# Kernel tuning notes

Measured on AMD Instinct MI355X. Metric: run time of the kernel, lower is better.

Reference implementation:

```python
import jax, jax.numpy as jnp
import numpy as np
import math

B, LL, LP, H, C, S, T = 16, 512, 2048, 1024, 8192, 10, 4
PAD_TOKEN_ID = 2000
VAR_TOKEN_BASE = 2001


def _attend(q, k, v):
    # q: [b,q,h], k/v: [b,k,h]
    scores = jnp.einsum('bqh,bkh->bqk', q, k) / math.sqrt(float(q.shape[-1]))
    w = jax.nn.softmax(scores, axis=-1)
    return jnp.einsum('bqk,bkh->bqh', w, v)


def _gru_cell(x, h, Wih, Whh, bih, bhh):
    gi = x @ Wih + bih   # [B,3H], gate order r,z,n (torch GRUCell)
    gh = h @ Whh + bhh
    i_r, i_z, i_n = jnp.split(gi, 3, axis=-1)
    h_r, h_z, h_n = jnp.split(gh, 3, axis=-1)
    r = jax.nn.sigmoid(i_r + h_r)
    z = jax.nn.sigmoid(i_z + h_z)
    n = jnp.tanh(i_n + r * h_n)
    return (1.0 - z) * n + z * h


def setup_inputs() -> dict:
    key = jax.random.key(0)
    ks = jax.random.split(key, 18)
    def lin(k, i, o):
        return jax.random.normal(k, (i, o), jnp.float32) * 0.02
    return {
        'logic_hidden': jax.random.normal(ks[0], (B, LL, H), jnp.float32),
        'prompt_hidden': jax.random.normal(ks[1], (B, LP, H), jnp.float32),
        'codebook_emb': jax.random.normal(ks[2], (C, H), jnp.float32) * 0.02,
        'W_init': lin(ks[3], 2 * H, H),
        'W_pq': lin(ks[4], H, H),
        'W_pk': lin(ks[5], H, H),
        'W_pv': lin(ks[6], H, H),
        'slot_queries': jax.random.normal(ks[7], (S - 1, H), jnp.float32) * 0.02,
        'W_sq': lin(ks[8], H, H),
        'W_op': lin(ks[9], H, H),
        'W_gate': lin(ks[10], H, 1),
        'b_gate': jnp.zeros((1,), jnp.float32),
        'W_stop': lin(ks[11], 2 * H, 1),
        'b_stop': jnp.zeros((1,), jnp.float32),
        'gru_Wih': lin(ks[12], H, 3 * H),
        'gru_Whh': lin(ks[13], H, 3 * H),
        'gru_bih': jnp.zeros((3 * H,), jnp.float32),
        'gru_bhh': jnp.zeros((3 * H,), jnp.float32),
    }


def reference(logic_hidden, prompt_hidden, codebook_emb, W_init, W_pq, W_pk, W_pv,
              slot_queries, W_sq, W_op, W_gate, b_gate, W_stop, b_stop,
              gru_Wih, gru_Whh, gru_bih, gru_bhh):
    batch = logic_hidden.shape[0]
    prompt_summary = prompt_hidden.mean(axis=1)
    logic_summary = logic_hidden.mean(axis=1)
    state = jnp.tanh(jnp.concatenate([prompt_summary, logic_summary], axis=-1) @ W_init)
    pk = prompt_hidden @ W_pk   # [B,LP,H]
    pv = prompt_hidden @ W_pv
    cb_sq = jnp.sum(codebook_emb * codebook_emb, axis=-1)   # [C]
    slot_idx = jnp.arange(S - 1, dtype=jnp.int64)[None, :].repeat(batch, axis=0)

    summaries, stop_logits, stop_probs = [], [], []
    for _ in range(T):
        state_q = (state @ W_pq)[:, None, :]
        state_ctx = _attend(state_q, pk, pv)[:, 0, :]         # [B,H]
        op_pre = state_ctx @ W_op
        # squared euclidean distance to codebook without [B,C,H] diff tensor
        dist = (jnp.sum(op_pre * op_pre, axis=-1, keepdims=True)
                - 2.0 * (op_pre @ codebook_emb.T) + cb_sq[None, :])  # [B,C]
        op_logits = -dist
        op_idx = jnp.argmax(op_logits, axis=-1)               # [B]
        op_embedding = codebook_emb[op_idx]                   # [B,H]
        slot_seed = state_ctx[:, None, :] + slot_queries[None, :, :]   # [B,S-1,H]
        slot_q = slot_seed @ W_sq
        slot_tensors = _attend(slot_q, pk, pv)                # [B,S-1,H]
        slot_use_probs = jax.nn.sigmoid((slot_seed @ W_gate)[..., 0] + b_gate[0])  # [B,S-1]
        slot_mask = slot_use_probs >= 0.5
        # fallback if no slot selected anywhere in the batch (global check, as in torch)
        fb_mask = jax.nn.one_hot(jnp.argmax(slot_use_probs, axis=-1), S - 1, dtype=jnp.bool_)
        slot_mask = jnp.where(jnp.any(slot_mask), slot_mask, fb_mask)
        mf = slot_mask.astype(slot_tensors.dtype)
        slot_summary = jnp.sum(slot_tensors * mf[..., None], axis=1) / \
            jnp.clip(jnp.sum(mf, axis=-1, keepdims=True), 1.0)
        matrix_summary = jnp.tanh(op_embedding + slot_summary)
        stop_logit = (jnp.concatenate([state_ctx, matrix_summary], axis=-1) @ W_stop)[:, 0] + b_stop[0]
        summaries.append(matrix_summary)
        stop_logits.append(stop_logit)
        stop_probs.append(jax.nn.sigmoid(stop_logit))
        state = _gru_cell(matrix_summary, state, gru_Wih, gru_Whh, gru_bih, gru_bhh)

    stop_logits_t = jnp.stack(stop_logits, axis=1)   # [B,T]
    stop_probs_t = jnp.stack(stop_probs, axis=1)
    summary_stack = jnp.stack(summaries, axis=1)     # [B,T,H]
    stop_hits = stop_probs_t >= 0.5
    chain_lengths = jnp.argmax(stop_hits.astype(jnp.int64), axis=1) + 1
    chain_lengths = jnp.where(jnp.sum(stop_hits, axis=1) == 0,
                              jnp.full_like(chain_lengths, T), chain_lengths)
    return summary_stack, stop_logits_t, stop_probs_t, chain_lengths
```

## Files before the change

kernel.cpp:

```cpp
#include <hip/hip_runtime.h>


#define DINL __device__ __forceinline__

DINL float dot4(float4 a, float4 b) {
  return fmaf(a.x, b.x, fmaf(a.y, b.y, fmaf(a.z, b.z, a.w * b.w)));
}
DINL unsigned sortable(float f) {
  unsigned u = __float_as_uint(f);
  return (u & 0x80000000u) ? ~u : (u | 0x80000000u);
}
#define AXPY4(A, W, P) \
  { A.x = fmaf(W, P.x, A.x); A.y = fmaf(W, P.y, A.y); A.z = fmaf(W, P.z, A.z); A.w = fmaf(W, P.w, A.w); }
#define ADD4(A, V) { A.x += V.x; A.y += V.y; A.z += V.z; A.w += V.w; }

static constexpr int F_CBSQ  = 0;
static constexpr int F_STATE = 8192;
static constexpr int F_WQK   = 24576;
static constexpr int F_T1    = F_WQK + 1048576;
static constexpr int F_WFUSE = F_T1 + 1048576;
static constexpr int F_SQKCP = F_WFUSE + 2105344;
static constexpr int F_E     = F_SQKCP + 36928;
static constexpr int F_UN    = F_E + 294912;
static constexpr int F_PMP   = F_UN;
static constexpr int F_LMP   = F_PMP + 1048576;
static constexpr int F_MEAN  = F_LMP + 262144;
static constexpr int F_S2P   = F_MEAN + 32768;
static constexpr int F_WQKP  = F_UN;
static constexpr int F_T1P   = F_UN + 4194304;
static constexpr int F_WFP   = F_UN;
static constexpr int F_QS1   = F_UN;
static constexpr int F_LST   = F_QS1 + 131072;
static constexpr int F_CTX   = F_LST + 4096;
static constexpr int F_FWP   = F_CTX + 16384;
static constexpr int F_OPV   = F_FWP + 1052672;
static constexpr int F_OPMAX = F_OPV + 16384;
static constexpr int F_OPIDX = F_OPMAX + 16384;
static constexpr int F_GPRE  = F_OPIDX + 64;
static constexpr int F_GC    = F_GPRE + 64;
static constexpr int F_STOPA = F_GC + 64;
static constexpr int F_QSLB  = F_STOPA + 64;
static constexpr int F_LPS   = F_QSLB + 16384;
static constexpr int F_SSUM  = F_LPS + 4672;
static constexpr int F_MS    = F_SSUM + 16384;
static constexpr int F_GP    = F_MS + 16384;
static constexpr int F_K8P   = F_GP + 786432;
static constexpr int F_BIG   = F_K8P + 262144;

struct SG {
  const float* Bm;
  const float* Bg;
  const float* a0;
  float* out;
  int M, N, Ncore, NB, kslice, ksh, lda, ldb, ldo, mr;
  float scale;
};

template <int MR>
DINL void sgemm_body(const SG p, int bx, float* As) {
  const int t = threadIdx.x;
  const int ks = bx / p.NB, nb = bx % p.NB;
  const int kslice = p.kslice;
  const int kb = ks * kslice;
  const int tot = p.M * kslice;
  for (int idx = t; idx < tot; idx += 256) {
    const int m = idx >> p.ksh;
    const int kl = idx & (kslice - 1);
    As[(m << p.ksh) + kl] = p.a0[m * p.lda + kb + kl];
  }
  __syncthreads();
  const int nl = t & 63, mg = t >> 6;
  const int n = nb * 64 + nl;
  const bool nok = (n < p.N);
  float acc[MR];
#pragma unroll
  for (int i = 0; i < MR; i++) acc[i] = 0.f;
  const bool useg = nok && (n >= p.Ncore);
  const float* Bc = p.Bm + n;
  for (int k4 = 0; k4 < kslice; k4 += 4) {
    float bv[4];
#pragma unroll
    for (int u = 0; u < 4; u++) {
      bv[u] = 0.f;
      if (nok) bv[u] = useg ? p.Bg[kb + k4 + u] : Bc[(kb + k4 + u) * p.ldb];
    }
#pragma unroll
    for (int i = 0; i < MR; i++) {
      const int m = mg + 4 * i;
      if (MR == 4 || m < p.M) {
        const float4 av = *(const float4*)&As[(m << p.ksh) + k4];
        acc[i] = fmaf(av.x, bv[0], acc[i]);
        acc[i] = fmaf(av.y, bv[1], acc[i]);
        acc[i] = fmaf(av.z, bv[2], acc[i]);
        acc[i] = fmaf(av.w, bv[3], acc[i]);
      }
    }
  }
  if (nok) {
#pragma unroll
    for (int i = 0; i < MR; i++) {
      const int m = mg + 4 * i;
      if (MR == 4 || m < p.M) p.out[(ks * p.M + m) * p.ldo + n] = acc[i] * p.scale;
    }
  }
}

__global__ __launch_bounds__(256) void k_sgemm(SG p) {
  __shared__ __align__(16) float As[4352];
  if (p.mr == 4) sgemm_body<4>(p, blockIdx.x, As);
  else sgemm_body<7>(p, blockIdx.x, As);
}

DINL int sw4(int c) { return c ^ (((c >> 5) & 3) << 2); }

__global__ __launch_bounds__(256) void k_wgT(const float* __restrict__ A1,
                                             const float* __restrict__ B,
                                             float* __restrict__ C1P,
                                             const float* __restrict__ A2,
                                             float* __restrict__ C2P) {
  __shared__ __align__(16) float As[16 * 132], Bs[16 * 132];
  const int bx = blockIdx.x;
  const int which = bx >> 8;
  const int rem = bx & 255;
  const int ks = rem >> 6;
  const int tile = rem & 63;
  const int bi = tile >> 3, bj = tile & 7;
  const float* A = which ? A2 : A1;
  float* CP = (which ? C2P : C1P) + ks * 1048576;
  const int t = threadIdx.x;
  const int sr = t >> 2, q4 = t & 3;
  const int tr = (t >> 4) << 3, tc = (t & 15) << 3;
  const int stc0 = sw4(tc), stc1 = sw4(tc + 4);
  float acc[8][8];
#pragma unroll
  for (int i = 0; i < 8; i++)
#pragma unroll
    for (int j = 0; j < 8; j++) acc[i][j] = 0.f;

  const int k00 = ks * 256;
  for (int k0 = k00; k0 < k00 + 256; k0 += 16) {
    __syncthreads();
#pragma unroll
    for (int h = 0; h < 2; h++) {
      const int r = sr + h * 64;
      const float4 av = *(const float4*)&A[(bi * 128 + r) * 1024 + k0 + q4 * 4];
      const float4 bv = *(const float4*)&B[(bj * 128 + r) * 1024 + k0 + q4 * 4];
      As[(q4 * 4 + 0) * 132 + r] = av.x; As[(q4 * 4 + 1) * 132 + r] = av.y;
      As[(q4 * 4 + 2) * 132 + r] = av.z; As[(q4 * 4 + 3) * 132 + r] = av.w;
      const int swr = sw4(r);
      Bs[(q4 * 4 + 0) * 132 + swr] = bv.x; Bs[(q4 * 4 + 1) * 132 + swr] = bv.y;
      Bs[(q4 * 4 + 2) * 132 + swr] = bv.z; Bs[(q4 * 4 + 3) * 132 + swr] = bv.w;
    }
    __syncthreads();
#pragma unroll
    for (int kk = 0; kk < 16; kk++) {
      const float* ar = &As[kk * 132];
      const float* br = &Bs[kk * 132];
      const float4 a0 = *(const float4*)&ar[tr];
      const float4 a1 = *(const float4*)&ar[tr + 4];
      const float4 b0 = *(const float4*)&br[stc0];
      const float4 b1 = *(const float4*)&br[stc1];
      const float a[8] = {a0.x, a0.y, a0.z, a0.w, a1.x, a1.y, a1.z, a1.w};
      const float b[8] = {b0.x, b0.y, b0.z, b0.w, b1.x, b1.y, b1.z, b1.w};
#pragma unroll
      for (int i = 0; i < 8; i++)
#pragma unroll
        for (int j = 0; j < 8; j++) acc[i][j] = fmaf(a[i], b[j], acc[i][j]);
    }
  }
#pragma unroll
  for (int i = 0; i < 8; i++) {
    const int row = bi * 128 + tr + i;
    *(float4*)&CP[row * 1024 + bj * 128 + tc] =
        make_float4(acc[i][0], acc[i][1], acc[i][2], acc[i][3]);
    *(float4*)&CP[row * 1024 + bj * 128 + tc + 4] =
        make_float4(acc[i][4], acc[i][5], acc[i][6], acc[i][7]);
  }
}

__global__ __launch_bounds__(256) void k_combT(const float* __restrict__ C1P,
                                               const float* __restrict__ C2P,
                                               float* __restrict__ C1,
                                               float* __restrict__ C2, float scale) {
  const int bx = blockIdx.x;
  const int half = bx >> 12;
  const int i = ((bx & 4095) << 8) + threadIdx.x;
  const float* src = half ? C2P : C1P;
  float s = 0.f;
#pragma unroll
  for (int ks = 0; ks < 4; ks++) s += src[ks * 1048576 + i];
  (half ? C2 : C1)[i] = s * scale;
}

__global__ __launch_bounds__(256) void k_wgF(const float* __restrict__ Wpv,
                                             const float* __restrict__ Wop,
                                             const float* __restrict__ T1,
                                             float* __restrict__ CfP) {
  __shared__ __align__(16) float As[16 * 132], Bs[16 * 132];
  const int bx = blockIdx.x;
  const int ks = bx >> 7;
  const int rem = bx & 127;
  const int bi = rem >> 4, bj = rem & 15;
  const float* Bsrc = (bj < 8) ? (Wop + bj * 128) : (T1 + (bj - 8) * 128);
  float* CP = CfP + ks * 2105344;
  const int t = threadIdx.x;
  const int sr = t >> 2, q4 = t & 3;
  const int kkq = t >> 4, c8 = (t & 15) << 3;
  const int tr = (t >> 4) << 3, tc = (t & 15) << 3;
  const int stc0 = sw4(tc), stc1 = sw4(tc + 4);
  float acc[8][8];
#pragma unroll
  for (int i = 0; i < 8; i++)
#pragma unroll
    for (int j = 0; j < 8; j++) acc[i][j] = 0.f;

  const int k00 = ks * 256;
  for (int k0 = k00; k0 < k00 + 256; k0 += 16) {
    __syncthreads();
#pragma unroll
    for (int h = 0; h < 2; h++) {
      const int r = sr + h * 64;
      const float4 av = *(const float4*)&Wpv[(bi * 128 + r) * 1024 + k0 + q4 * 4];
      As[(q4 * 4 + 0) * 132 + r] = av.x; As[(q4 * 4 + 1) * 132 + r] = av.y;
      As[(q4 * 4 + 2) * 132 + r] = av.z; As[(q4 * 4 + 3) * 132 + r] = av.w;
    }
    {
      const float4 v0 = *(const float4*)&Bsrc[(k0 + kkq) * 1024 + c8];
      const float4 v1 = *(const float4*)&Bsrc[(k0 + kkq) * 1024 + c8 + 4];
      *(float4*)&Bs[kkq * 132 + sw4(c8)] = v0;
      *(float4*)&Bs[kkq * 132 + sw4(c8 + 4)] = v1;
    }
    __syncthreads();
#pragma unroll
    for (int kk = 0; kk < 16; kk++) {
      const float* ar = &As[kk * 132];
      const float* br = &Bs[kk * 132];
      const float4 a0 = *(const float4*)&ar[tr];
      const float4 a1 = *(const float4*)&ar[tr + 4];
      const float4 b0 = *(const float4*)&br[stc0];
      const float4 b1 = *(const float4*)&br[stc1];
      const float a[8] = {a0.x, a0.y, a0.z, a0.w, a1.x, a1.y, a1.z, a1.w};
      const float b[8] = {b0.x, b0.y, b0.z, b0.w, b1.x, b1.y, b1.z, b1.w};
#pragma unroll
      for (int i = 0; i < 8; i++)
#pragma unroll
        for (int j = 0; j < 8; j++) acc[i][j] = fmaf(a[i], b[j], acc[i][j]);
    }
  }
#pragma unroll
  for (int i = 0; i < 8; i++) {
    const int row = bi * 128 + tr + i;
    *(float4*)&CP[row * 2056 + bj * 128 + tc] =
        make_float4(acc[i][0], acc[i][1], acc[i][2], acc[i][3]);
    *(float4*)&CP[row * 2056 + bj * 128 + tc + 4] =
        make_float4(acc[i][4], acc[i][5], acc[i][6], acc[i][7]);
  }
}

__global__ __launch_bounds__(256) void k_combF(const float* __restrict__ CfP,
                                               float* __restrict__ Cf) {
  const int i2 = blockIdx.x * 256 + threadIdx.x;
  const int r = i2 >> 11, c = i2 & 2047;
  float s = 0.f;
#pragma unroll
  for (int ks = 0; ks < 4; ks++) s += CfP[ks * 2105344 + r * 2056 + c];
  Cf[r * 2056 + c] = s;
}

__global__ __launch_bounds__(256) void k_gs(const float* __restrict__ Wpv,
                                            const float* __restrict__ Wgate,
                                            const float* __restrict__ Wstop,
                                            float* __restrict__ Cf) {
  const int t = threadIdx.x;
  const int row = blockIdx.x * 16 + (t >> 4);
  const int lane = t & 15;
  const float* base = Wpv + row * 1024 + lane * 64;
  const float* gb = Wgate + lane * 64;
  const float* sb = Wstop + lane * 64;
  float g = 0.f, s = 0.f;
#pragma unroll 4
  for (int k = 0; k < 64; k += 4) {
    const float4 av = *(const float4*)&base[k];
    const float4 gv = *(const float4*)&gb[k];
    const float4 sv = *(const float4*)&sb[k];
    g += dot4(av, gv);
    s += dot4(av, sv);
  }
#pragma unroll
  for (int off = 8; off > 0; off >>= 1) {
    g += __shfl_xor(g, off);
    s += __shfl_xor(s, off);
  }
  if (lane == 0) {
    Cf[row * 2056 + 2048] = g;
    Cf[row * 2056 + 2049] = s;
  }
}

__global__ __launch_bounds__(512) void k_E(const float* __restrict__ prompt,
                                           const float* __restrict__ sqkcP,
                                           float* __restrict__ E) {
  __shared__ __align__(16) char qsm[36864];
  const int b = blockIdx.y, kc = blockIdx.x;
  const int t = threadIdx.x;
  for (int idx = t; idx < 9216; idx += 512) {
    const int j = idx >> 10, h = idx & 1023;
    float s = 0.f;
    for (int sp = 0; sp < 4; sp++) s += sqkcP[(sp * 9 + j) * 1025 + h];
    const int x = idx << 2;
    *(float*)(qsm + (x ^ (((x >> 7) & 7) << 4))) = s;
  }
  __syncthreads();
  const int w = t >> 6, l = t & 63;
  const int bxl = 64 * l;
  const int key = ((bxl >> 7) & 7) << 4;
  const int o0 = bxl ^ key, o1 = (bxl + 16) ^ key, o2 = (bxl + 32) ^ key, o3 = (bxl + 48) ^ key;
  const int k0 = kc * 64 + w * 8;
  const float* pbase = prompt + ((b * 2048 + k0) << 10) + 16 * l;
  for (int ki = 0; ki < 8; ki++) {
    const float4* pr = (const float4*)(pbase + (ki << 10));
    const float4 p0 = pr[0], p1 = pr[1], p2 = pr[2], p3 = pr[3];
    float sj[9];
#pragma unroll
    for (int j = 0; j < 9; j++) {
      const char* qp = qsm + (j << 12);
      sj[j] = dot4(*(const float4*)(qp + o0), p0) + dot4(*(const float4*)(qp + o1), p1) +
              dot4(*(const float4*)(qp + o2), p2) + dot4(*(const float4*)(qp + o3), p3);
    }
#pragma unroll
    for (int off = 32; off > 0; off >>= 1) {
#pragma unroll
      for (int j = 0; j < 9; j++) sj[j] += __shfl_xor(sj[j], off);
    }
    float wv = sj[0];
#pragma unroll
    for (int j = 1; j < 9; j++)
      if (l == j) wv = sj[j];
    if (l < 9) E[(b * 2048 + k0 + ki) * 9 + l] = __expf(wv);
  }
}

__global__ __launch_bounds__(256) void k_meanpsum(const float* __restrict__ src,
                                                  float* __restrict__ out, int rpc) {
  const int s = blockIdx.x, b = blockIdx.y, t = threadIdx.x;
  const int R = gridDim.x * rpc;
  const float4* base = (const float4*)src + (size_t)(b * R + s * rpc) * 256 + t;
  float4 acc = make_float4(0.f, 0.f, 0.f, 0.f);
#pragma unroll 4
  for (int r = 0; r < rpc; r++) {
    const float4 v = base[r * 256];
    ADD4(acc, v);
  }
  ((float4*)out)[((s * 16 + b) << 8) + t] = acc;
}

__global__ __launch_bounds__(256) void k_cbsq(const float* __restrict__ cbv,
                                              float* __restrict__ out) {
  const int c = blockIdx.x * 4 + (threadIdx.x >> 6);
  const int l = threadIdx.x & 63;
  const float4* cr = (const float4*)(cbv + (c << 10));
  float s = 0.f;
#pragma unroll
  for (int r = 0; r < 4; r++) {
    const float4 v = cr[4 * l + r];
    s += dot4(v, v);
  }
#pragma unroll
  for (int off = 32; off > 0; off >>= 1) s += __shfl_xor(s, off);
  if (l == 0) out[c] = s;
}

__global__ __launch_bounds__(256) void k_meancat(const float* __restrict__ pmp,
                                                 const float* __restrict__ lmp,
                                                 float* __restrict__ mean) {
  const int gi = blockIdx.x * 256 + threadIdx.x;
  const int b = gi >> 11, k = gi & 2047;
  float v = 0.f;
  if (k < 1024) {
    for (int s = 0; s < 64; s++) v += pmp[((s * 16 + b) << 10) + k];
    v *= (1.f / 2048.f);
  } else {
    const int kk = k - 1024;
    for (int s = 0; s < 16; s++) v += lmp[((s * 16 + b) << 10) + kk];
    v *= (1.f / 512.f);
  }
  mean[b * 2048 + k] = v;
}

__global__ __launch_bounds__(256) void k_s2b(const float* __restrict__ s2p,
                                             float* __restrict__ state) {
  const int gi = blockIdx.x * 256 + threadIdx.x;
  const int b = gi >> 10, h = gi & 1023;
  float s = 0.f;
  for (int si = 0; si < 8; si++) s += s2p[((si * 16 + b) << 10) + h];
  state[gi] = tanhf(s);
}


DINL void ph_qs1(int bx, char* smemc, const float* state, const float* Wqk,
                 float* outP) {
  float* As = (float*)smemc;
  const int t = threadIdx.x;
  const int ks = bx >> 4, nb = bx & 15;
  const int kb = ks * 128;
  for (int idx = t; idx < 2048; idx += 256)
    As[idx] = state[((idx >> 7) << 10) + kb + (idx & 127)];
  __syncthreads();
  const int nl = t & 63, mg = t >> 6;
  const int n = nb * 64 + nl;
  const float* Bc = Wqk + n;
  float acc[4] = {0.f, 0.f, 0.f, 0.f};
  for (int k4 = 0; k4 < 128; k4 += 4) {
    float bv[4];
#pragma unroll
    for (int u = 0; u < 4; u++) bv[u] = Bc[(kb + k4 + u) << 10];
#pragma unroll
    for (int i = 0; i < 4; i++) {
      const float4 av = *(const float4*)&As[((mg + 4 * i) << 7) + k4];
      acc[i] = fmaf(av.x, bv[0], acc[i]);
      acc[i] = fmaf(av.y, bv[1], acc[i]);
      acc[i] = fmaf(av.z, bv[2], acc[i]);
      acc[i] = fmaf(av.w, bv[3], acc[i]);
    }
  }
#pragma unroll
  for (int i = 0; i < 4; i++)
    outP[((ks * 16 + mg + 4 * i) << 10) + n] = acc[i];
}

DINL void ph_flash(int vb, const float* prompt, const float* qs1P,
                   float* accst, float* lst) {
  const int b = vb >> 6;
  const int w = threadIdx.x >> 6, l = threadIdx.x & 63;
  const int chunk = (vb & 63) * 4 + w;
  float4 q0 = make_float4(0.f, 0.f, 0.f, 0.f), q1 = q0, q2 = q0, q3 = q0;
#pragma unroll
  for (int s = 0; s < 8; s++) {
    const float4* qp = (const float4*)(qs1P + ((s * 16 + b) << 10) + 16 * l);
    ADD4(q0, qp[0]); ADD4(q1, qp[1]); ADD4(q2, qp[2]); ADD4(q3, qp[3]);
  }
  float4 acc[4];
#pragma unroll
  for (int r = 0; r < 4; r++) acc[r] = make_float4(0.f, 0.f, 0.f, 0.f);
  float lsum = 0.f;
  const float* pbase = prompt + ((b * 2048 + chunk * 8) << 10) + 16 * l;
#pragma unroll 2
  for (int k = 0; k < 8; k++) {
    const float4* pr = (const float4*)(pbase + (k << 10));
    const float4 p0 = pr[0], p1 = pr[1], p2 = pr[2], p3 = pr[3];
    float s = dot4(q0, p0) + dot4(q1, p1) + dot4(q2, p2) + dot4(q3, p3);
#pragma unroll
    for (int off = 32; off > 0; off >>= 1) s += __shfl_xor(s, off);
    const float wgt = __expf(s);
    lsum += wgt;
    AXPY4(acc[0], wgt, p0); AXPY4(acc[1], wgt, p1);
    AXPY4(acc[2], wgt, p2); AXPY4(acc[3], wgt, p3);
  }
  float* ob = accst + ((chunk * 16 + b) << 10) + 16 * l;
#pragma unroll
  for (int r = 0; r < 4; r++) ((float4*)ob)[r] = acc[r];
  if (l == 0) lst[chunk * 16 + b] = lsum;
}

DINL void ph_cst(int bx, char* smemc, const float* accst, const float* lst,
                 float* ctx) {
  float4* sred = (float4*)smemc;
  float* rinvp = (float*)(smemc + 4096);
  const int b = bx >> 4, hq = bx & 15;
  const int t = threadIdx.x;
  if (t < 64) {
    float s = 0.f;
    for (int c = t; c < 256; c += 64) s += lst[c * 16 + b];
#pragma unroll
    for (int off = 32; off > 0; off >>= 1) s += __shfl_xor(s, off);
    if (t == 0) rinvp[0] = 1.f / s;
  }
  const int h4 = hq * 16 + (t & 15);
  const int cp = t >> 4;
  float4 a = make_float4(0.f, 0.f, 0.f, 0.f);
#pragma unroll
  for (int ci = 0; ci < 16; ci++) {
    const int c = cp * 16 + ci;
    const float4 v = ((const float4*)accst)[((c * 16 + b) << 8) + h4];
    ADD4(a, v);
  }
  sred[t] = a;
  __syncthreads();
  if (t < 16) {
    float4 s = sred[t];
    for (int p2 = 1; p2 < 16; p2++) {
      const float4 v = sred[p2 * 16 + t];
      ADD4(s, v);
    }
    const float rinv = rinvp[0];
    s.x *= rinv; s.y *= rinv; s.z *= rinv; s.w *= rinv;
    ((float4*)ctx)[(b << 8) + hq * 16 + t] = s;
  }
}

DINL void ph_fw(int bx, char* smemc, const float* ctx, const float* wfuse,
                float* outp) {
  float* As = (float*)smemc;
  const int t = threadIdx.x;
  const int ks = bx / 33, nb = bx % 33;
  const int kb = ks * 64;
  for (int idx = t; idx < 1024; idx += 256)
    As[idx] = ctx[((idx >> 6) << 10) + kb + (idx & 63)];
  __syncthreads();
  const int nl = t & 63, mg = t >> 6;
  const int n = nb * 64 + nl;
  const bool nok = (n < 2050);
  const float* Bc = wfuse + n;
  float acc[4] = {0.f, 0.f, 0.f, 0.f};
  for (int k4 = 0; k4 < 64; k4 += 4) {
    float bv[4];
#pragma unroll
    for (int u = 0; u < 4; u++) bv[u] = nok ? Bc[(kb + k4 + u) * 2056] : 0.f;
#pragma unroll
    for (int i = 0; i < 4; i++) {
      const float4 av = *(const float4*)&As[((mg + 4 * i) << 6) + k4];
      acc[i] = fmaf(av.x, bv[0], acc[i]);
      acc[i] = fmaf(av.y, bv[1], acc[i]);
      acc[i] = fmaf(av.z, bv[2], acc[i]);
      acc[i] = fmaf(av.w, bv[3], acc[i]);
    }
  }
  if (nok) {
#pragma unroll
    for (int i = 0; i < 4; i++) outp[(ks * 16 + mg + 4 * i) * 2056 + n] = acc[i];
  }
}

DINL void ph_combw(int bx, const float* fwP, const float* sqkcP, float* opv,
                   float* qslb, float* gpre, float* gc, float* stopA) {
  const int t = threadIdx.x;
  if (bx < 64) {
    const int i = bx * 256 + t;
    const int b = i >> 10, h = i & 1023;
    float s = 0.f;
    for (int p = 0; p < 16; p++) s += fwP[(p * 16 + b) * 2056 + h];
    opv[i] = s;
  } else if (bx < 128) {
    const int i = (bx - 64) * 256 + t;
    const int b = i >> 10, h = i & 1023;
    float s = 0.f;
    for (int p = 0; p < 16; p++) s += fwP[(p * 16 + b) * 2056 + 1024 + h];
    qslb[i] = s;
  } else {
    if (t < 16) {
      float g = 0.f, sa = 0.f;
      for (int p = 0; p < 16; p++) {
        g += fwP[(p * 16 + t) * 2056 + 2048];
        sa += fwP[(p * 16 + t) * 2056 + 2049];
      }
      gpre[t] = g;
      stopA[t] = sa;
    } else if (t < 25) {
      const int j = t - 16;
      float g = 0.f;
      for (int sp = 0; sp < 4; sp++) g += sqkcP[(sp * 9 + j) * 1025 + 1024];
      gc[j] = g;
    }
  }
}

DINL void ph_slot(int vb, char* smemc, const float* prompt, const float* qslb,
                  const float* E, float* accp, float* lpsum) {
  float* wl = (float*)smemc;
  float* lred = (float*)(smemc + 2560);
  const int kc = vb & 31, b = vb >> 5;
  const int t = threadIdx.x;
  const int w = t >> 6, l = t & 63;
  const float4* qp = (const float4*)(qslb + (b << 10) + 16 * l);
  const float4 q0 = qp[0], q1 = qp[1], q2 = qp[2], q3 = qp[3];
  const int kbase = kc * 64 + w * 16;
  float lacc = 0.f;
  const float* pbase = prompt + ((b * 2048 + kbase) << 10) + 16 * l;
  for (int ki = 0; ki < 16; ki++) {
    const float4* pr = (const float4*)(pbase + (ki << 10));
    const float4 p0 = pr[0], p1 = pr[1], p2 = pr[2], p3 = pr[3];
    float s = dot4(q0, p0) + dot4(q1, p1) + dot4(q2, p2) + dot4(q3, p3);
#pragma unroll
    for (int off = 32; off > 0; off >>= 1) s += __shfl_xor(s, off);
    const float we = __expf(s);
    if (l < 9) {
      const float wv = we * E[(b * 2048 + kbase + ki) * 9 + l];
      wl[(w * 16 + ki) * 10 + l] = wv;
      lacc += wv;
    }
  }
  if (l < 9) lred[w * 9 + l] = lacc;
  __syncthreads();
  if (t < 9)
    lpsum[(b * 32 + kc) * 9 + t] = lred[t] + lred[9 + t] + lred[18 + t] + lred[27 + t];
  const int h4 = (w << 8) + (l << 2);
  float4 acc[9];
#pragma unroll
  for (int j = 0; j < 9; j++) acc[j] = make_float4(0.f, 0.f, 0.f, 0.f);
  const float* pb2 = prompt + ((b * 2048 + kc * 64) << 10) + h4;
#pragma unroll 2
  for (int k = 0; k < 64; k++) {
    const float4 pv = *(const float4*)(pb2 + (k << 10));
    const float* wr = &wl[k * 10];
#pragma unroll
    for (int j = 0; j < 9; j++) AXPY4(acc[j], wr[j], pv);
  }
  float* ob = accp + (((kc * 16 + b) * 9) << 10) + h4;
#pragma unroll
  for (int j = 0; j < 9; j++) *(float4*)(ob + (j << 10)) = acc[j];
}

DINL void ph_cb(int vb, char* smemc, const float* opv, const float* cbv,
                const float* cbsqv, unsigned long long* opmaxp) {
  const int t = threadIdx.x;
  const int w = t >> 6, l = t & 63;
  const int bxl = 64 * l;
  const int key = ((bxl >> 7) & 7) << 4;
  const int o0 = bxl ^ key, o1 = (bxl + 16) ^ key, o2 = (bxl + 32) ^ key, o3 = (bxl + 48) ^ key;
  for (int half = 0; half < 2; half++) {
    __syncthreads();
    for (int idx = t; idx < 8192; idx += 256) {
      const int x = idx << 2;
      *(float*)(smemc + (x ^ (((x >> 7) & 7) << 4))) = opv[half * 8192 + idx];
    }
    __syncthreads();
    unsigned long long bk[8];
#pragma unroll
    for (int m = 0; m < 8; m++) bk[m] = 0ull;
    const int cbase = (vb << 4) + (w << 2);
    for (int ci = 0; ci < 4; ci++) {
      const int c = cbase + ci;
      const float4* cr = (const float4*)(cbv + (c << 10));
      const float4 c0 = cr[4 * l], c1 = cr[4 * l + 1], c2 = cr[4 * l + 2], c3 = cr[4 * l + 3];
      float sm[8];
#pragma unroll
      for (int m = 0; m < 8; m++) {
        const char* qp = smemc + (m << 12);
        const float4 a0 = *(const float4*)(qp + o0);
        const float4 a1 = *(const float4*)(qp + o1);
        const float4 a2 = *(const float4*)(qp + o2);
        const float4 a3 = *(const float4*)(qp + o3);
        sm[m] = dot4(a0, c0) + dot4(a1, c1) + dot4(a2, c2) + dot4(a3, c3);
      }
#pragma unroll
      for (int off = 32; off > 0; off >>= 1) {
#pragma unroll
        for (int m = 0; m < 8; m++) sm[m] += __shfl_xor(sm[m], off);
      }
      const float cq = cbsqv[c];
#pragma unroll
      for (int m = 0; m < 8; m++) {
        const float sc = fmaf(2.f, sm[m], -cq);
        const unsigned long long k2 =
            ((unsigned long long)sortable(sc) << 32) | (unsigned)(8192 - c);
        bk[m] = k2 > bk[m] ? k2 : bk[m];
      }
    }
    unsigned long long* red = (unsigned long long*)(smemc + 32768);
    __syncthreads();
    if (l == 0) {
#pragma unroll
      for (int m = 0; m < 8; m++) red[w * 8 + m] = bk[m];
    }
    __syncthreads();
    if (t < 8) {
      unsigned long long b2 = red[t];
      for (int ww = 1; ww < 4; ww++) {
        const unsigned long long v = red[ww * 8 + t];
        b2 = v > b2 ? v : b2;
      }
      opmaxp[vb * 16 + half * 8 + t] = b2;
    }
  }
}

DINL void ph_k7(int bx, char* smemc, const float* accp, const float* lpsum,
                const float* gpre_g, const float* gc_g, const float* bgate,
                const unsigned long long* opmax, int* opidx, float* ssum) {
  unsigned long long* red = (unsigned long long*)smemc;
  float* rl = (float*)(smemc + 2048);
  float* gpre = (float*)(smemc + 2112);
  float* gcs = (float*)(smemc + 2192);
  int* mask_s = (int*)(smemc + 2240);
  float* cntInvp = (float*)(smemc + 2288);
  const int t = threadIdx.x;
  if (bx == 64) {
    const int b = t & 15, part = t >> 4;
    unsigned long long best = 0ull;
    for (int c = part * 32; c < part * 32 + 32; c++) {
      const unsigned long long v = opmax[c * 16 + b];
      best = v > best ? v : best;
    }
    red[t] = best;
    __syncthreads();
    if (t < 16) {
      unsigned long long m = red[t];
      for (int p2 = 1; p2 < 16; p2++) {
        const unsigned long long v = red[p2 * 16 + t];
        m = v > m ? v : m;
      }
      opidx[t] = 8192 - (int)(unsigned)(m & 0xFFFFFFFFull);
    }
    return;
  }
  const int b = bx >> 2;
  if (t < 9) {
    float s = 0.f;
    for (int c = 0; c < 32; c++) s += lpsum[(b * 32 + c) * 9 + t];
    rl[t] = 1.f / s;
  }
  if (t >= 32 && t < 48) gpre[t - 32] = gpre_g[t - 32];
  if (t >= 48 && t < 57) gcs[t - 48] = gc_g[t - 48];
  __syncthreads();
  if (t == 0) {
    const float bg = bgate[0];
    bool any = false;
    for (int bb = 0; bb < 16; bb++)
      for (int j = 0; j < 9; j++)
        if (gpre[bb] + gcs[j] + bg >= 0.f) any = true;
    int cnt = 0;
    if (any) {
      for (int j = 0; j < 9; j++) {
        const int s = (gpre[b] + gcs[j] + bg >= 0.f) ? 1 : 0;
        mask_s[j] = s;
        cnt += s;
      }
    } else {
      float bv = -3.4e38f;
      int bj = 0;
      for (int j = 0; j < 9; j++) {
        const float v = gpre[b] + gcs[j] + bg;
        if (v > bv) { bv = v; bj = j; }
      }
      for (int j = 0; j < 9; j++) mask_s[j] = (j == bj) ? 1 : 0;
      cnt = 1;
    }
    cntInvp[0] = 1.f / (float)(cnt > 0 ? cnt : 1);
  }
  __syncthreads();
  const int h = ((bx & 3) << 8) + t;
  float v = 0.f;
  for (int j = 0; j < 9; j++) {
    if (mask_s[j]) {
      float s = 0.f;
      for (int c = 0; c < 32; c++) s += accp[(((c * 16 + b) * 9 + j) << 10) + h];
      v = fmaf(s, rl[j], v);
    }
  }
  ssum[(b << 10) + h] = v * cntInvp[0];
}

DINL void ph_k8p(int bx, char* smemc, const float* ssum, const float* Wpv,
                 float* outP) {
  float* As = (float*)smemc;
  const int t = threadIdx.x;
  const int ks = bx >> 4, nb = bx & 15;
  const int kb = ks * 64;
  for (int idx = t; idx < 1024; idx += 256)
    As[idx] = ssum[((idx >> 6) << 10) + kb + (idx & 63)];
  __syncthreads();
  const int nl = t & 63, mg = t >> 6;
  const int n = nb * 64 + nl;
  const float* Bc = Wpv + n;
  float acc[4] = {0.f, 0.f, 0.f, 0.f};
  for (int k4 = 0; k4 < 64; k4 += 4) {
    float bv[4];
#pragma unroll
    for (int u = 0; u < 4; u++) bv[u] = Bc[(kb + k4 + u) << 10];
#pragma unroll
    for (int i = 0; i < 4; i++) {
      const float4 av = *(const float4*)&As[((mg + 4 * i) << 6) + k4];
      acc[i] = fmaf(av.x, bv[0], acc[i]);
      acc[i] = fmaf(av.y, bv[1], acc[i]);
      acc[i] = fmaf(av.z, bv[2], acc[i]);
      acc[i] = fmaf(av.w, bv[3], acc[i]);
    }
  }
#pragma unroll
  for (int i = 0; i < 4; i++)
    outP[((ks * 16 + mg + 4 * i) << 10) + n] = acc[i];
}

DINL void ph_gru(int bx, char* smemc, const float* k8p, const int* opidx,
                 const float* cbv, const float* state, const float* Wih,
                 const float* Whh, float* gpP, float* ms, float* dout, int it) {
  float* As = (float*)smemc;
  const int t = threadIdx.x;
  const int half = (bx >= 384) ? 1 : 0;
  const int b2 = half ? bx - 384 : bx;
  const int ks = b2 / 48, nb = b2 % 48;
  const int kb = ks * 128;
  for (int idx = t; idx < 2048; idx += 256) {
    const int m = idx >> 7, kl = idx & 127;
    float v;
    if (!half) {
      float s = 0.f;
      for (int p = 0; p < 16; p++) s += k8p[((p * 16 + m) << 10) + kb + kl];
      v = tanhf(s + cbv[(opidx[m] << 10) + kb + kl]);
      if (nb == 0) {
        ms[(m << 10) + kb + kl] = v;
        dout[(m << 12) + (it << 10) + kb + kl] = v;
      }
    } else {
      v = state[(m << 10) + kb + kl];
    }
    As[idx] = v;
  }
  __syncthreads();
  const int nl = t & 63, mg = t >> 6;
  const int n = nb * 64 + nl;
  const float* Bc = (half ? Whh : Wih) + n;
  float acc[4] = {0.f, 0.f, 0.f, 0.f};
  for (int k4 = 0; k4 < 128; k4 += 4) {
    float bv[4];
#pragma unroll
    for (int u = 0; u < 4; u++) bv[u] = Bc[(kb + k4 + u) * 3072];
#pragma unroll
    for (int i = 0; i < 4; i++) {
      const float4 av = *(const float4*)&As[((mg + 4 * i) << 7) + k4];
      acc[i] = fmaf(av.x, bv[0], acc[i]);
      acc[i] = fmaf(av.y, bv[1], acc[i]);
      acc[i] = fmaf(av.z, bv[2], acc[i]);
      acc[i] = fmaf(av.w, bv[3], acc[i]);
    }
  }
  float* outp = gpP + half * 3072;
#pragma unroll
  for (int i = 0; i < 4; i++) outp[(ks * 16 + mg + 4 * i) * 6144 + n] = acc[i];
}

DINL void ph_k9b(int bx, const float* gp, const float* bih, const float* bhh,
                 float* state, const float* stopA, const float* ms,
                 const float* Wstop, const float* bstop, float* dout, int it) {
  const int t = threadIdx.x;
  if (bx < 64) {
    const int gi = bx * 256 + t;
    const int b = gi >> 10, h = gi & 1023;
    float ir = 0.f, iz = 0.f, inn = 0.f, hr = 0.f, hz = 0.f, hn = 0.f;
    for (int s = 0; s < 8; s++) {
      const float* g = gp + (s * 16 + b) * 6144;
      ir += g[h]; iz += g[1024 + h]; inn += g[2048 + h];
      hr += g[3072 + h]; hz += g[4096 + h]; hn += g[5120 + h];
    }
    ir += bih[h]; iz += bih[1024 + h]; inn += bih[2048 + h];
    hr += bhh[h]; hz += bhh[1024 + h]; hn += bhh[2048 + h];
    const float r = 1.f / (1.f + __expf(-(ir + hr)));
    const float z = 1.f / (1.f + __expf(-(iz + hz)));
    const float n = tanhf(fmaf(r, hn, inn));
    const float hold = state[gi];
    state[gi] = (1.f - z) * n + z * hold;
  } else {
    const int wid = (bx - 64) * 4 + (t >> 6);
    const int l = t & 63;
    float p = 0.f;
    for (int i = 0; i < 16; i++) {
      const int h = l + (i << 6);
      p = fmaf(ms[(wid << 10) + h], Wstop[1024 + h], p);
    }
#pragma unroll
    for (int off = 32; off > 0; off >>= 1) p += __shfl_xor(p, off);
    if (l == 0) {
      const float lg = p + stopA[wid] + bstop[0];
      dout[65536 + wid * 4 + it] = lg;
      dout[65600 + wid * 4 + it] = 1.f / (1.f + __expf(-lg));
    }
  }
}

__global__ __launch_bounds__(256) void kf_qs1(const float* state, const float* Wqk, float* outP) {
  __shared__ __align__(16) char smem[8192];
  ph_qs1(blockIdx.x, smem, state, Wqk, outP);
}
__global__ __launch_bounds__(256) void kf_flash(const float* prompt, const float* qs1P,
                                                float* accst, float* lst) {
  ph_flash(blockIdx.x, prompt, qs1P, accst, lst);
}
__global__ __launch_bounds__(256) void kf_cst(const float* accst, const float* lst, float* ctx) {
  __shared__ __align__(16) char smem[4112];
  ph_cst(blockIdx.x, smem, accst, lst, ctx);
}
__global__ __launch_bounds__(256) void kf_fw(const float* ctx, const float* wfuse, float* outp) {
  __shared__ __align__(16) char smem[4096];
  ph_fw(blockIdx.x, smem, ctx, wfuse, outp);
}
__global__ __launch_bounds__(256) void kf_combw(const float* fwP, const float* sqkcP,
                                                float* opv, float* qslb, float* gpre,
                                                float* gc, float* stopA) {
  ph_combw(blockIdx.x, fwP, sqkcP, opv, qslb, gpre, gc, stopA);
}
__global__ __launch_bounds__(256) void k_slotcb(const float* prompt, const float* qslb,
                                                const float* E, float* accp, float* lpsum,
                                                const float* opv, const float* cbv,
                                                const float* cbsqv,
                                                unsigned long long* opmaxp) {
  __shared__ __align__(16) char smem[33024];
  const int bx = blockIdx.x;
  if (bx < 512) ph_slot(bx, smem, prompt, qslb, E, accp, lpsum);
  else ph_cb(bx - 512, smem, opv, cbv, cbsqv, opmaxp);
}
__global__ __launch_bounds__(256) void kf_k7(const float* accp, const float* lpsum,
                                             const float* gpre_g, const float* gc_g,
                                             const float* bgate,
                                             const unsigned long long* opmax,
                                             int* opidx, float* ssum) {
  __shared__ __align__(16) char smem[2304];
  ph_k7(blockIdx.x, smem, accp, lpsum, gpre_g, gc_g, bgate, opmax, opidx, ssum);
}
__global__ __launch_bounds__(256) void kf_k8p(const float* ssum, const float* Wpv, float* outP) {
  __shared__ __align__(16) char smem[4096];
  ph_k8p(blockIdx.x, smem, ssum, Wpv, outP);
}
__global__ __launch_bounds__(256) void kf_gru(const float* k8p, const int* opidx,
                                              const float* cbv, const float* state,
                                              const float* Wih, const float* Whh,
                                              float* gpP, float* ms, float* dout, int it) {
  __shared__ __align__(16) char smem[8192];
  ph_gru(blockIdx.x, smem, k8p, opidx, cbv, state, Wih, Whh, gpP, ms, dout, it);
}
__global__ __launch_bounds__(256) void kf_k9b(const float* gp, const float* bih,
                                              const float* bhh, float* state,
                                              const float* stopA, const float* ms,
                                              const float* Wstop, const float* bstop,
                                              float* dout, int it) {
  ph_k9b(blockIdx.x, gp, bih, bhh, state, stopA, ms, Wstop, bstop, dout, it);
}
__global__ void kf_k10(float* __restrict__ dout) {
  const int t = threadIdx.x;
  if (t < 16) {
    int cl = 4;
    for (int it = 0; it < 4; it++) {
      if (dout[65536 + t * 4 + it] >= 0.f) { cl = it + 1; break; }
    }
    dout[65664 + t] = (float)cl;
  }
}

static SG baseSG() {
  SG p;
  p.Bm = nullptr; p.Bg = nullptr; p.a0 = nullptr; p.out = nullptr;
  p.M = 16; p.N = 1024; p.Ncore = 1024;
  p.NB = 16; p.kslice = 64; p.ksh = 6;
  p.lda = 1024; p.ldb = 1024; p.ldo = 1024;
  p.mr = 4; p.scale = 1.f;
  return p;
}

extern "C" void kernel_launch(void* const* d_in, const int* in_sizes, int n_in,
                              void* d_out, int out_size, void* d_ws, size_t ws_size,
                              hipStream_t stream) {
  (void)in_sizes; (void)n_in; (void)out_size; (void)ws_size;
  const float* logic  = (const float*)d_in[0];
  const float* prompt = (const float*)d_in[1];
  const float* cbv    = (const float*)d_in[2];
  const float* W_init = (const float*)d_in[3];
  const float* W_pq   = (const float*)d_in[4];
  const float* W_pk   = (const float*)d_in[5];
  const float* W_pv   = (const float*)d_in[6];
  const float* slotq  = (const float*)d_in[7];
  const float* W_sq   = (const float*)d_in[8];
  const float* W_op   = (const float*)d_in[9];
  const float* W_gate = (const float*)d_in[10];
  const float* b_gate = (const float*)d_in[11];
  const float* W_stop = (const float*)d_in[12];
  const float* b_stop = (const float*)d_in[13];
  const float* Wih    = (const float*)d_in[14];
  const float* Whh    = (const float*)d_in[15];
  const float* bih    = (const float*)d_in[16];
  const float* bhh    = (const float*)d_in[17];
  float* out = (float*)d_out;
  float* w = (float*)d_ws;

  const float inv32 = 1.0f / 32.0f;

  k_meanpsum<<<dim3(64, 16), 256, 0, stream>>>(prompt, w + F_PMP, 32);
  k_meanpsum<<<dim3(16, 16), 256, 0, stream>>>(logic, w + F_LMP, 32);
  k_cbsq<<<2048, 256, 0, stream>>>(cbv, w + F_CBSQ);
  k_gs<<<64, 256, 0, stream>>>(W_pv, W_gate, W_stop, w + F_WFUSE);
  k_meancat<<<128, 256, 0, stream>>>(w + F_PMP, w + F_LMP, w + F_MEAN);
  {
    SG p = baseSG();
    p.a0 = w + F_MEAN; p.Bm = W_init; p.out = w + F_S2P;
    p.kslice = 256; p.ksh = 8; p.lda = 2048; p.NB = 16;
    k_sgemm<<<128, 256, 0, stream>>>(p);
  }
  k_s2b<<<64, 256, 0, stream>>>(w + F_S2P, w + F_STATE);
  k_wgT<<<512, 256, 0, stream>>>(W_pq, W_pk, w + F_WQKP, W_sq, w + F_T1P);
  k_combT<<<8192, 256, 0, stream>>>(w + F_WQKP, w + F_T1P, w + F_WQK, w + F_T1, inv32);
  {
    SG p = baseSG();
    p.a0 = slotq; p.Bm = w + F_T1; p.Bg = W_gate;
    p.M = 9; p.N = 1025; p.Ncore = 1024; p.NB = 17;
    p.kslice = 256; p.ksh = 8; p.out = w + F_SQKCP; p.ldo = 1025; p.mr = 7;
    k_sgemm<<<68, 256, 0, stream>>>(p);
  }
  k_E<<<dim3(32, 16), 512, 0, stream>>>(prompt, w + F_SQKCP, w + F_E);
  k_wgF<<<512, 256, 0, stream>>>(W_pv, W_op, w + F_T1, w + F_WFP);
  k_combF<<<8192, 256, 0, stream>>>(w + F_WFP, w + F_WFUSE);

  for (int it = 0; it < 4; ++it) {
    kf_qs1<<<128, 256, 0, stream>>>(w + F_STATE, w + F_WQK, w + F_QS1);
    kf_flash<<<1024, 256, 0, stream>>>(prompt, w + F_QS1, w + F_BIG, w + F_LST);
    kf_cst<<<256, 256, 0, stream>>>(w + F_BIG, w + F_LST, w + F_CTX);
    kf_fw<<<528, 256, 0, stream>>>(w + F_CTX, w + F_WFUSE, w + F_FWP);
    kf_combw<<<129, 256, 0, stream>>>(w + F_FWP, w + F_SQKCP, w + F_OPV,
                                      w + F_QSLB, w + F_GPRE, w + F_GC, w + F_STOPA);
    k_slotcb<<<1024, 256, 0, stream>>>(prompt, w + F_QSLB, w + F_E,
                                       w + F_BIG, w + F_LPS, w + F_OPV, cbv,
                                       w + F_CBSQ,
                                       (unsigned long long*)(w + F_OPMAX));
    kf_k7<<<65, 256, 0, stream>>>(w + F_BIG, w + F_LPS, w + F_GPRE, w + F_GC,
                                  b_gate, (const unsigned long long*)(w + F_OPMAX),
                                  (int*)(w + F_OPIDX), w + F_SSUM);
    kf_k8p<<<256, 256, 0, stream>>>(w + F_SSUM, W_pv, w + F_K8P);
    kf_gru<<<768, 256, 0, stream>>>(w + F_K8P, (const int*)(w + F_OPIDX), cbv,
                                    w + F_STATE, Wih, Whh, w + F_GP, w + F_MS,
                                    out, it);
    kf_k9b<<<68, 256, 0, stream>>>(w + F_GP, bih, bhh, w + F_STATE, w + F_STOPA,
                                   w + F_MS, W_stop, b_stop, out, it);
  }
  kf_k10<<<1, 64, 0, stream>>>(out);
}
```

Measured before the change: 900.9 us.

## Fold flash and combine reductions into consumer kernels, dropping two launches per step

The flash kernel now reduces its four waves' partial accumulators in shared memory and writes one partial per 32-key group. The context reduction and normalisation move into the fused-weight GEMM's A-tile load, replacing the separate ctx kernel. The split-K combine kernel is removed: slot queries, op vectors, gate and stop terms are summed from the split-K partials inside each consumer. The codebook scan uses fewer, larger blocks (16 codes per wave). This cuts two launches per iteration and some intermediate traffic, at the cost of redundant partial sums in consumers, notably 64-way reads per A element in the fw blocks and 16-way sums repeated in every cb block.

```diff
diff --git a/kernel.cpp b/kernel.cpp
--- a/kernel.cpp
+++ b/kernel.cpp
@@ -30,17 +30,12 @@
 static constexpr int F_T1P   = F_UN + 4194304;
 static constexpr int F_WFP   = F_UN;
 static constexpr int F_QS1   = F_UN;
-static constexpr int F_LST   = F_QS1 + 131072;
-static constexpr int F_CTX   = F_LST + 4096;
-static constexpr int F_FWP   = F_CTX + 16384;
-static constexpr int F_OPV   = F_FWP + 1052672;
-static constexpr int F_OPMAX = F_OPV + 16384;
-static constexpr int F_OPIDX = F_OPMAX + 16384;
-static constexpr int F_GPRE  = F_OPIDX + 64;
-static constexpr int F_GC    = F_GPRE + 64;
-static constexpr int F_STOPA = F_GC + 64;
-static constexpr int F_QSLB  = F_STOPA + 64;
-static constexpr int F_LPS   = F_QSLB + 16384;
+static constexpr int F_ACCSM = F_QS1 + 131072;
+static constexpr int F_LSM   = F_ACCSM + 1048576;
+static constexpr int F_FWP   = F_LSM + 1024;
+static constexpr int F_OPMAX = F_FWP + 526336;
+static constexpr int F_OPIDX = F_OPMAX + 4096;
+static constexpr int F_LPS   = F_OPIDX + 64;
 static constexpr int F_SSUM  = F_LPS + 4672;
 static constexpr int F_MS    = F_SSUM + 16384;
 static constexpr int F_GP    = F_MS + 16384;
@@ -428,11 +423,12 @@
     outP[((ks * 16 + mg + 4 * i) << 10) + n] = acc[i];
 }
 
-DINL void ph_flash(int vb, const float* prompt, const float* qs1P,
-                   float* accst, float* lst) {
-  const int b = vb >> 6;
-  const int w = threadIdx.x >> 6, l = threadIdx.x & 63;
-  const int chunk = (vb & 63) * 4 + w;
+DINL void ph_flash(int g, int b, char* smemc, const float* prompt,
+                   const float* qs1P, float* accsm, float* lsm) {
+  float* red = (float*)smemc;
+  float* lred = (float*)(smemc + 16384);
+  const int t = threadIdx.x;
+  const int w = t >> 6, l = t & 63;
   float4 q0 = make_float4(0.f, 0.f, 0.f, 0.f), q1 = q0, q2 = q0, q3 = q0;
 #pragma unroll
   for (int s = 0; s < 8; s++) {
@@ -443,7 +439,8 @@
 #pragma unroll
   for (int r = 0; r < 4; r++) acc[r] = make_float4(0.f, 0.f, 0.f, 0.f);
   float lsum = 0.f;
-  const float* pbase = prompt + ((b * 2048 + chunk * 8) << 10) + 16 * l;
+  const int k0 = g * 32 + w * 8;
+  const float* pbase = prompt + ((b * 2048 + k0) << 10) + 16 * l;
 #pragma unroll 2
   for (int k = 0; k < 8; k++) {
     const float4* pr = (const float4*)(pbase + (k << 10));
@@ -456,56 +453,39 @@
     AXPY4(acc[0], wgt, p0); AXPY4(acc[1], wgt, p1);
     AXPY4(acc[2], wgt, p2); AXPY4(acc[3], wgt, p3);
   }
-  float* ob = accst + ((chunk * 16 + b) << 10) + 16 * l;
-#pragma unroll
-  for (int r = 0; r < 4; r++) ((float4*)ob)[r] = acc[r];
-  if (l == 0) lst[chunk * 16 + b] = lsum;
-}
-
-DINL void ph_cst(int bx, char* smemc, const float* accst, const float* lst,
-                 float* ctx) {
-  float4* sred = (float4*)smemc;
-  float* rinvp = (float*)(smemc + 4096);
-  const int b = bx >> 4, hq = bx & 15;
-  const int t = threadIdx.x;
-  if (t < 64) {
-    float s = 0.f;
-    for (int c = t; c < 256; c += 64) s += lst[c * 16 + b];
-#pragma unroll
-    for (int off = 32; off > 0; off >>= 1) s += __shfl_xor(s, off);
-    if (t == 0) rinvp[0] = 1.f / s;
-  }
-  const int h4 = hq * 16 + (t & 15);
-  const int cp = t >> 4;
-  float4 a = make_float4(0.f, 0.f, 0.f, 0.f);
-#pragma unroll
-  for (int ci = 0; ci < 16; ci++) {
-    const int c = cp * 16 + ci;
-    const float4 v = ((const float4*)accst)[((c * 16 + b) << 8) + h4];
-    ADD4(a, v);
-  }
-  sred[t] = a;
-  __syncthreads();
-  if (t < 16) {
-    float4 s = sred[t];
-    for (int p2 = 1; p2 < 16; p2++) {
-      const float4 v = sred[p2 * 16 + t];
-      ADD4(s, v);
-    }
-    const float rinv = rinvp[0];
-    s.x *= rinv; s.y *= rinv; s.z *= rinv; s.w *= rinv;
-    ((float4*)ctx)[(b << 8) + hq * 16 + t] = s;
-  }
-}
-
-DINL void ph_fw(int bx, char* smemc, const float* ctx, const float* wfuse,
-                float* outp) {
+  float4* myr = (float4*)(red + w * 1024 + 16 * l);
+  myr[0] = acc[0]; myr[1] = acc[1]; myr[2] = acc[2]; myr[3] = acc[3];
+  if (l == 0) lred[w] = lsum;
+  __syncthreads();
+  float4 s0 = *(float4*)(red + t * 4);
+  const float4 s1 = *(float4*)(red + 1024 + t * 4);
+  const float4 s2 = *(float4*)(red + 2048 + t * 4);
+  const float4 s3 = *(float4*)(red + 3072 + t * 4);
+  ADD4(s0, s1); ADD4(s0, s2); ADD4(s0, s3);
+  *(float4*)&accsm[((b * 64 + g) << 10) + t * 4] = s0;
+  if (t == 0) lsm[b * 64 + g] = lred[0] + lred[1] + lred[2] + lred[3];
+}
+
+DINL void ph_fw(int bx, char* smemc, const float* accsm, const float* lsm,
+                const float* wfuse, float* outp) {
   float* As = (float*)smemc;
+  float* rl = (float*)(smemc + 4096);
   const int t = threadIdx.x;
   const int ks = bx / 33, nb = bx % 33;
   const int kb = ks * 64;
-  for (int idx = t; idx < 1024; idx += 256)
-    As[idx] = ctx[((idx >> 6) << 10) + kb + (idx & 63)];
+  if (t < 16) {
+    float s = 0.f;
+    for (int g = 0; g < 64; g++) s += lsm[t * 64 + g];
+    rl[t] = 1.f / s;
+  }
+  __syncthreads();
+  for (int idx = t; idx < 1024; idx += 256) {
+    const int m = idx >> 6;
+    const int h = kb + (idx & 63);
+    float s = 0.f;
+    for (int g = 0; g < 64; g++) s += accsm[((m * 64 + g) << 10) + h];
+    As[idx] = s * rl[m];
+  }
   __syncthreads();
   const int nl = t & 63, mg = t >> 6;
   const int n = nb * 64 + nl;
@@ -531,48 +511,19 @@
   }
 }
 
-DINL void ph_combw(int bx, const float* fwP, const float* sqkcP, float* opv,
-                   float* qslb, float* gpre, float* gc, float* stopA) {
-  const int t = threadIdx.x;
-  if (bx < 64) {
-    const int i = bx * 256 + t;
-    const int b = i >> 10, h = i & 1023;
-    float s = 0.f;
-    for (int p = 0; p < 16; p++) s += fwP[(p * 16 + b) * 2056 + h];
-    opv[i] = s;
-  } else if (bx < 128) {
-    const int i = (bx - 64) * 256 + t;
-    const int b = i >> 10, h = i & 1023;
-    float s = 0.f;
-    for (int p = 0; p < 16; p++) s += fwP[(p * 16 + b) * 2056 + 1024 + h];
-    qslb[i] = s;
-  } else {
-    if (t < 16) {
-      float g = 0.f, sa = 0.f;
-      for (int p = 0; p < 16; p++) {
-        g += fwP[(p * 16 + t) * 2056 + 2048];
-        sa += fwP[(p * 16 + t) * 2056 + 2049];
-      }
-      gpre[t] = g;
-      stopA[t] = sa;
-    } else if (t < 25) {
-      const int j = t - 16;
-      float g = 0.f;
-      for (int sp = 0; sp < 4; sp++) g += sqkcP[(sp * 9 + j) * 1025 + 1024];
-      gc[j] = g;
-    }
-  }
-}
-
-DINL void ph_slot(int vb, char* smemc, const float* prompt, const float* qslb,
+DINL void ph_slot(int vb, char* smemc, const float* prompt, const float* fwP,
                   const float* E, float* accp, float* lpsum) {
   float* wl = (float*)smemc;
   float* lred = (float*)(smemc + 2560);
   const int kc = vb & 31, b = vb >> 5;
   const int t = threadIdx.x;
   const int w = t >> 6, l = t & 63;
-  const float4* qp = (const float4*)(qslb + (b << 10) + 16 * l);
-  const float4 q0 = qp[0], q1 = qp[1], q2 = qp[2], q3 = qp[3];
+  float4 q0 = make_float4(0.f, 0.f, 0.f, 0.f), q1 = q0, q2 = q0, q3 = q0;
+#pragma unroll 4
+  for (int p = 0; p < 16; p++) {
+    const float4* qp = (const float4*)&fwP[(p * 16 + b) * 2056 + 1024 + 16 * l];
+    ADD4(q0, qp[0]); ADD4(q1, qp[1]); ADD4(q2, qp[2]); ADD4(q3, qp[3]);
+  }
   const int kbase = kc * 64 + w * 16;
   float lacc = 0.f;
   const float* pbase = prompt + ((b * 2048 + kbase) << 10) + 16 * l;
@@ -610,7 +561,7 @@
   for (int j = 0; j < 9; j++) *(float4*)(ob + (j << 10)) = acc[j];
 }
 
-DINL void ph_cb(int vb, char* smemc, const float* opv, const float* cbv,
+DINL void ph_cb(int vb, char* smemc, const float* fwP, const float* cbv,
                 const float* cbsqv, unsigned long long* opmaxp) {
   const int t = threadIdx.x;
   const int w = t >> 6, l = t & 63;
@@ -620,15 +571,19 @@
   for (int half = 0; half < 2; half++) {
     __syncthreads();
     for (int idx = t; idx < 8192; idx += 256) {
+      const int gi = half * 8192 + idx;
+      const int b2 = gi >> 10, h = gi & 1023;
+      float s = 0.f;
+      for (int p = 0; p < 16; p++) s += fwP[(p * 16 + b2) * 2056 + h];
       const int x = idx << 2;
-      *(float*)(smemc + (x ^ (((x >> 7) & 7) << 4))) = opv[half * 8192 + idx];
+      *(float*)(smemc + (x ^ (((x >> 7) & 7) << 4))) = s;
     }
     __syncthreads();
     unsigned long long bk[8];
 #pragma unroll
     for (int m = 0; m < 8; m++) bk[m] = 0ull;
-    const int cbase = (vb << 4) + (w << 2);
-    for (int ci = 0; ci < 4; ci++) {
+    const int cbase = (vb << 6) + (w << 4);
+    for (int ci = 0; ci < 16; ci++) {
       const int c = cbase + ci;
       const float4* cr = (const float4*)(cbv + (c << 10));
       const float4 c0 = cr[4 * l], c1 = cr[4 * l + 1], c2 = cr[4 * l + 2], c3 = cr[4 * l + 3];
@@ -675,7 +630,7 @@
 }
 
 DINL void ph_k7(int bx, char* smemc, const float* accp, const float* lpsum,
-                const float* gpre_g, const float* gc_g, const float* bgate,
+                const float* fwP, const float* sqkcP, const float* bgate,
                 const unsigned long long* opmax, int* opidx, float* ssum) {
   unsigned long long* red = (unsigned long long*)smemc;
   float* rl = (float*)(smemc + 2048);
@@ -687,7 +642,7 @@
   if (bx == 64) {
     const int b = t & 15, part = t >> 4;
     unsigned long long best = 0ull;
-    for (int c = part * 32; c < part * 32 + 32; c++) {
+    for (int c = part * 8; c < part * 8 + 8; c++) {
       const unsigned long long v = opmax[c * 16 + b];
       best = v > best ? v : best;
     }
@@ -709,8 +664,16 @@
     for (int c = 0; c < 32; c++) s += lpsum[(b * 32 + c) * 9 + t];
     rl[t] = 1.f / s;
   }
-  if (t >= 32 && t < 48) gpre[t - 32] = gpre_g[t - 32];
-  if (t >= 48 && t < 57) gcs[t - 48] = gc_g[t - 48];
+  if (t >= 32 && t < 48) {
+    float g = 0.f;
+    for (int p = 0; p < 16; p++) g += fwP[(p * 16 + (t - 32)) * 2056 + 2048];
+    gpre[t - 32] = g;
+  }
+  if (t >= 48 && t < 57) {
+    float g = 0.f;
+    for (int sp = 0; sp < 4; sp++) g += sqkcP[(sp * 9 + (t - 48)) * 1025 + 1024];
+    gcs[t - 48] = g;
+  }
   __syncthreads();
   if (t == 0) {
     const float bg = bgate[0];
@@ -830,7 +793,7 @@
 }
 
 DINL void ph_k9b(int bx, const float* gp, const float* bih, const float* bhh,
-                 float* state, const float* stopA, const float* ms,
+                 float* state, const float* fwP, const float* ms,
                  const float* Wstop, const float* bstop, float* dout, int it) {
   const int t = threadIdx.x;
   if (bx < 64) {
@@ -860,7 +823,9 @@
 #pragma unroll
     for (int off = 32; off > 0; off >>= 1) p += __shfl_xor(p, off);
     if (l == 0) {
-      const float lg = p + stopA[wid] + bstop[0];
+      float sa = 0.f;
+      for (int pp = 0; pp < 16; pp++) sa += fwP[(pp * 16 + wid) * 2056 + 2049];
+      const float lg = p + sa + bstop[0];
       dout[65536 + wid * 4 + it] = lg;
       dout[65600 + wid * 4 + it] = 1.f / (1.f + __expf(-lg));
     }
@@ -872,39 +837,31 @@
   ph_qs1(blockIdx.x, smem, state, Wqk, outP);
 }
 __global__ __launch_bounds__(256) void kf_flash(const float* prompt, const float* qs1P,
-                                                float* accst, float* lst) {
-  ph_flash(blockIdx.x, prompt, qs1P, accst, lst);
-}
-__global__ __launch_bounds__(256) void kf_cst(const float* accst, const float* lst, float* ctx) {
-  __shared__ __align__(16) char smem[4112];
-  ph_cst(blockIdx.x, smem, accst, lst, ctx);
-}
-__global__ __launch_bounds__(256) void kf_fw(const float* ctx, const float* wfuse, float* outp) {
-  __shared__ __align__(16) char smem[4096];
-  ph_fw(blockIdx.x, smem, ctx, wfuse, outp);
-}
-__global__ __launch_bounds__(256) void kf_combw(const float* fwP, const float* sqkcP,
-                                                float* opv, float* qslb, float* gpre,
-                                                float* gc, float* stopA) {
-  ph_combw(blockIdx.x, fwP, sqkcP, opv, qslb, gpre, gc, stopA);
-}
-__global__ __launch_bounds__(256) void k_slotcb(const float* prompt, const float* qslb,
+                                                float* accsm, float* lsm) {
+  __shared__ __align__(16) char smem[16416];
+  ph_flash(blockIdx.x, blockIdx.y, smem, prompt, qs1P, accsm, lsm);
+}
+__global__ __launch_bounds__(256) void kf_fw(const float* accsm, const float* lsm,
+                                             const float* wfuse, float* outp) {
+  __shared__ __align__(16) char smem[4160];
+  ph_fw(blockIdx.x, smem, accsm, lsm, wfuse, outp);
+}
+__global__ __launch_bounds__(256) void k_slotcb(const float* prompt, const float* fwP,
                                                 const float* E, float* accp, float* lpsum,
-                                                const float* opv, const float* cbv,
-                                                const float* cbsqv,
+                                                const float* cbv, const float* cbsqv,
                                                 unsigned long long* opmaxp) {
   __shared__ __align__(16) char smem[33024];
   const int bx = blockIdx.x;
-  if (bx < 512) ph_slot(bx, smem, prompt, qslb, E, accp, lpsum);
-  else ph_cb(bx - 512, smem, opv, cbv, cbsqv, opmaxp);
+  if (bx < 512) ph_slot(bx, smem, prompt, fwP, E, accp, lpsum);
+  else ph_cb(bx - 512, smem, fwP, cbv, cbsqv, opmaxp);
 }
 __global__ __launch_bounds__(256) void kf_k7(const float* accp, const float* lpsum,
-                                             const float* gpre_g, const float* gc_g,
+                                             const float* fwP, const float* sqkcP,
                                              const float* bgate,
                                              const unsigned long long* opmax,
                                              int* opidx, float* ssum) {
   __shared__ __align__(16) char smem[2304];
-  ph_k7(blockIdx.x, smem, accp, lpsum, gpre_g, gc_g, bgate, opmax, opidx, ssum);
+  ph_k7(blockIdx.x, smem, accp, lpsum, fwP, sqkcP, bgate, opmax, opidx, ssum);
 }
 __global__ __launch_bounds__(256) void kf_k8p(const float* ssum, const float* Wpv, float* outP) {
   __shared__ __align__(16) char smem[4096];
@@ -919,10 +876,10 @@
 }
 __global__ __launch_bounds__(256) void kf_k9b(const float* gp, const float* bih,
                                               const float* bhh, float* state,
-                                              const float* stopA, const float* ms,
+                                              const float* fwP, const float* ms,
                                               const float* Wstop, const float* bstop,
                                               float* dout, int it) {
-  ph_k9b(blockIdx.x, gp, bih, bhh, state, stopA, ms, Wstop, bstop, dout, it);
+  ph_k9b(blockIdx.x, gp, bih, bhh, state, fwP, ms, Wstop, bstop, dout, it);
 }
 __global__ void kf_k10(float* __restrict__ dout) {
   const int t = threadIdx.x;
@@ -999,23 +956,20 @@
 
   for (int it = 0; it < 4; ++it) {
     kf_qs1<<<128, 256, 0, stream>>>(w + F_STATE, w + F_WQK, w + F_QS1);
-    kf_flash<<<1024, 256, 0, stream>>>(prompt, w + F_QS1, w + F_BIG, w + F_LST);
-    kf_cst<<<256, 256, 0, stream>>>(w + F_BIG, w + F_LST, w + F_CTX);
-    kf_fw<<<528, 256, 0, stream>>>(w + F_CTX, w + F_WFUSE, w + F_FWP);
-    kf_combw<<<129, 256, 0, stream>>>(w + F_FWP, w + F_SQKCP, w + F_OPV,
-                                      w + F_QSLB, w + F_GPRE, w + F_GC, w + F_STOPA);
-    k_slotcb<<<1024, 256, 0, stream>>>(prompt, w + F_QSLB, w + F_E,
-                                       w + F_BIG, w + F_LPS, w + F_OPV, cbv,
-                                       w + F_CBSQ,
-                                       (unsigned long long*)(w + F_OPMAX));
-    kf_k7<<<65, 256, 0, stream>>>(w + F_BIG, w + F_LPS, w + F_GPRE, w + F_GC,
+    kf_flash<<<dim3(64, 16), 256, 0, stream>>>(prompt, w + F_QS1,
+                                               w + F_ACCSM, w + F_LSM);
+    kf_fw<<<528, 256, 0, stream>>>(w + F_ACCSM, w + F_LSM, w + F_WFUSE, w + F_FWP);
+    k_slotcb<<<640, 256, 0, stream>>>(prompt, w + F_FWP, w + F_E,
+                                      w + F_BIG, w + F_LPS, cbv, w + F_CBSQ,
+                                      (unsigned long long*)(w + F_OPMAX));
+    kf_k7<<<65, 256, 0, stream>>>(w + F_BIG, w + F_LPS, w + F_FWP, w + F_SQKCP,
                                   b_gate, (const unsigned long long*)(w + F_OPMAX),
                                   (int*)(w + F_OPIDX), w + F_SSUM);
     kf_k8p<<<256, 256, 0, stream>>>(w + F_SSUM, W_pv, w + F_K8P);
     kf_gru<<<768, 256, 0, stream>>>(w + F_K8P, (const int*)(w + F_OPIDX), cbv,
                                     w + F_STATE, Wih, Whh, w + F_GP, w + F_MS,
                                     out, it);
-    kf_k9b<<<68, 256, 0, stream>>>(w + F_GP, bih, bhh, w + F_STATE, w + F_STOPA,
+    kf_k9b<<<68, 256, 0, stream>>>(w + F_GP, bih, bhh, w + F_STATE, w + F_FWP,
                                    w + F_MS, W_stop, b_stop, out, it);
   }
   kf_k10<<<1, 64, 0, stream>>>(out);
```

After: 1.102 ms. +22.3%, slower.
